# Performance work log

Measured on AMD Instinct MI355X. Metric: run time of the kernel, lower is better.

Reference implementation:

```python
import jax, jax.numpy as jnp
from jax import lax
import numpy as np

B, C, H, W = 8, 192, 56, 56
N = H * W
K_CLUSTERS = 16   # num_centroids
K_NBRS = 9        # kNN neighbors
FACTOR = 2
COUT = C * FACTOR # hidden channels of graph conv
CPE_K = 7         # depthwise CPE kernel (odd)


def setup_inputs() -> dict:
    key = jax.random.key(0)
    ks = jax.random.split(key, 12)
    s = 0.02
    return {
        "x": jax.random.normal(ks[0], (B, C, H, W), jnp.float32),
        "labels": jax.random.randint(ks[1], (B, N), 0, K_CLUSTERS, jnp.int32),
        "cpe_w": jax.random.normal(ks[2], (C, 1, CPE_K, CPE_K), jnp.float32) * s,
        "cpe_b": jnp.zeros((C,), jnp.float32),
        "fc1_w": jax.random.normal(ks[3], (C, C), jnp.float32) * s,
        "fc1_b": jnp.zeros((C,), jnp.float32),
        "nn_v_w": jax.random.normal(ks[4], (2 * C, COUT), jnp.float32) * s,
        "nn_v_b": jnp.zeros((COUT,), jnp.float32),
        "nn_c_w": jax.random.normal(ks[5], (2 * C, COUT), jnp.float32) * s,
        "nn_c_b": jnp.zeros((COUT,), jnp.float32),
        "fc2_w": jax.random.normal(ks[6], (COUT, C), jnp.float32) * s,
        "fc2_b": jnp.zeros((C,), jnp.float32),
    }


def reference(x, labels, cpe_w, cpe_b, fc1_w, fc1_b, nn_v_w, nn_v_b,
              nn_c_w, nn_c_b, fc2_w, fc2_b):
    Bx, Cx, Hx, Wx = x.shape
    n = Hx * Wx
    shortcut = x
    # --- Conditional Position Encoding: depthwise conv + residual ---
    pe = lax.conv_general_dilated(
        x, cpe_w, (1, 1), "SAME", feature_group_count=Cx,
        dimension_numbers=("NCHW", "OIHW", "NCHW"))
    x = pe + cpe_b[None, :, None, None] + x
    # --- fc1: 1x1 conv ---
    xf = jnp.einsum("bchw,cd->bdhw", x, fc1_w) + fc1_b[None, :, None, None]
    xn = xf.reshape(Bx, Cx, n).transpose(0, 2, 1)  # [B,N,C]
    # --- organize_and_map: stable sort nodes by cluster label ---
    order = jnp.argsort(labels, axis=1)            # sorted pos -> orig idx (stable)
    mapping = jnp.argsort(order, axis=1)           # orig idx -> sorted pos
    xs = jnp.take_along_axis(xn, order[:, :, None], axis=1)  # [B,N,C]
    ls = jnp.take_along_axis(labels, order, axis=1)          # [B,N]
    # --- kNN on l2-normalized feats, restricted to same cluster ---
    xe = xs / jnp.maximum(jnp.linalg.norm(xs, axis=-1, keepdims=True), 1e-12)
    sq = jnp.sum(xe * xe, axis=-1)                 # [B,N]
    d2 = sq[:, :, None] + sq[:, None, :] - 2.0 * jnp.einsum("bnc,bmc->bnm", xe, xe)
    same = ls[:, :, None] == ls[:, None, :]        # [B,N,N] cluster mask
    d2 = jnp.where(same, d2, jnp.inf)
    _, nbr = lax.top_k(-d2, K_NBRS)                # [B,N,k] nearest in-cluster
    valid = jnp.take_along_axis(same, nbr, axis=2) # False when cluster < k
    # --- vertex edge conv: max_j MLP([x_i, x_j - x_i]) ---
    xj = jax.vmap(lambda xb, nb: xb[nb])(xs, nbr)  # [B,N,k,C]
    xi = xs[:, :, None, :]
    msg = jnp.concatenate([jnp.broadcast_to(xi, xj.shape), xj - xi], axis=-1)
    h = jax.nn.gelu(msg @ nn_v_w + nn_v_b)         # [B,N,k,COUT]
    h = jnp.where(valid[..., None], h, -jnp.inf)   # self is always valid
    hv = jnp.max(h, axis=2)                        # [B,N,COUT]
    # --- centroid edge conv over cluster centers (fully connected per image) ---
    onehot = (ls[:, :, None] == jnp.arange(K_CLUSTERS)[None, None, :]).astype(xs.dtype)
    cnt = jnp.maximum(onehot.sum(axis=1), 1.0)     # [B,K]
    cen = jnp.einsum("bnk,bnc->bkc", onehot, xs) / cnt[:, :, None]
    ci = cen[:, :, None, :]
    cj = cen[:, None, :, :]
    cmsg = jnp.concatenate(
        [jnp.broadcast_to(ci, (Bx, K_CLUSTERS, K_CLUSTERS, Cx)), cj - ci], axis=-1)
    hc = jnp.max(jax.nn.gelu(cmsg @ nn_c_w + nn_c_b), axis=2)  # [B,K,COUT]
    hcn = jax.vmap(lambda hb, lb: hb[lb])(hc, ls)  # scatter center feat to nodes
    hn = hv + hcn                                  # [B,N,COUT]
    # --- unshuffle back to original raster order ---
    out_nodes = jnp.take_along_axis(hn, mapping[:, :, None], axis=1)
    # --- fc2: 1x1 conv back to C, residual ---
    y = out_nodes @ fc2_w + fc2_b                  # [B,N,C]
    y = y.transpose(0, 2, 1).reshape(Bx, Cx, Hx, Wx)
    return y + shortcut
```

## Files before the change

### kernel.cpp

```cpp
#include <hip/hip_runtime.h>
#include <math.h>

#define NB 8
#define NC 192
#define NH 56
#define NW 56
#define NN 3136
#define NK 16
#define KNB 9
#define NCOUT 384
#define LPMAX 320
#define DSTRIDE 320
#define DSLOT (320 * 320)

#define FLT_INF __builtin_inff()

typedef short s16x8 __attribute__((ext_vector_type(8)));
typedef _Float16 f16x8 __attribute__((ext_vector_type(8)));
typedef float f32x4 __attribute__((ext_vector_type(4)));
typedef unsigned short us8 __attribute__((ext_vector_type(8)));
typedef unsigned short us4 __attribute__((ext_vector_type(4)));

__device__ __forceinline__ float gelu_t(float x) {
    const float k0 = 0.7978845608028654f;
    float u = k0 * (x + 0.044715f * x * x * x);
    float sg = __builtin_amdgcn_rcpf(1.0f + __expf(-2.0f * u));
    return x * sg;
}

__device__ __forceinline__ unsigned short f2bf(float f) {
    unsigned u = __float_as_uint(f);
    u += 0x7fff + ((u >> 16) & 1);
    return (unsigned short)(u >> 16);
}

__device__ __forceinline__ float bf2f(unsigned short h) {
    return __uint_as_float(((unsigned)h) << 16);
}


#define FRONT_CONV_BLOCKS (NB * NC)
#define FRONT_ORDER_BLOCKS (NB * NK)
#define FRONT_WCVT_BLOCKS 288
__global__ __launch_bounds__(256) void front_kernel(
    const float* __restrict__ X, const float* __restrict__ W7, const float* __restrict__ bias,
    unsigned short* __restrict__ xpe,
    const int* __restrict__ labels, int* __restrict__ order, int* __restrict__ mapping,
    int* __restrict__ lsv, int* __restrict__ cntk, int* __restrict__ offk,
    const float* __restrict__ Wf1, const float* __restrict__ Wv, const float* __restrict__ Wf2,
    unsigned short* __restrict__ wf1, unsigned short* __restrict__ wfpmq,
    unsigned short* __restrict__ wfq, unsigned short* __restrict__ wf2) {
    __shared__ float tile[62 * 62];
    __shared__ float wl[49];
    int bid = blockIdx.x;
    int tid = threadIdx.x;
    if (bid < FRONT_CONV_BLOCKS) {
        int bc = (bid & 7) * NC + (bid >> 3);
        int c = bc % NC;
        const float* Xp = X + (size_t)bc * NN;
        if (tid < 49) wl[tid] = W7[(size_t)c * 49 + tid];
        for (int idx = tid; idx < 62 * 62; idx += 256) {
            int ty = idx / 62, tx = idx % 62;
            int gy = ty - 3, gx = tx - 3;
            float v = 0.0f;
            if (gy >= 0 && gy < NH && gx >= 0 && gx < NW) v = Xp[gy * NW + gx];
            tile[idx] = v;
        }
        __syncthreads();
        float cb = bias[c];
        for (int g = tid; g < (NN / 4); g += 256) {
            int y = g / (NW / 4), x0 = (g % (NW / 4)) * 4;
            float a0 = 0.f, a1 = 0.f, a2 = 0.f, a3 = 0.f;
#pragma unroll
            for (int dy = 0; dy < 7; ++dy) {
                const float* tr = &tile[(y + dy) * 62 + x0];
#pragma unroll
                for (int dx = 0; dx < 7; ++dx) {
                    float wv = wl[dy * 7 + dx];
                    a0 += tr[dx] * wv;
                    a1 += tr[dx + 1] * wv;
                    a2 += tr[dx + 2] * wv;
                    a3 += tr[dx + 3] * wv;
                }
            }
            const float* rr = &tile[(y + 3) * 62 + x0 + 3];
            us4 o;
            o[0] = f2bf(a0 + cb + rr[0]);
            o[1] = f2bf(a1 + cb + rr[1]);
            o[2] = f2bf(a2 + cb + rr[2]);
            o[3] = f2bf(a3 + cb + rr[3]);
            *(us4*)(xpe + (size_t)bc * NN + y * NW + x0) = o;
        }
    } else if (bid < FRONT_CONV_BLOCKS + FRONT_ORDER_BLOCKS) {
        if (tid >= 64) return;
        int idx = bid - FRONT_CONV_BLOCKS;
        int b = idx >> 4;
        int k = idx & 15;
        int lane = tid;
        const int* lb = labels + (size_t)b * NN;
        int cntLess = 0, cntEq = 0;
        for (int n0 = 0; n0 < NN; n0 += 64) {
            int lab = lb[n0 + lane] & 15;
            cntLess += __popcll(__ballot(lab < k));
            cntEq += __popcll(__ballot(lab == k));
        }
        int base = cntLess;
        int run = 0;
        for (int n0 = 0; n0 < NN; n0 += 64) {
            int n = n0 + lane;
            int lab = lb[n] & 15;
            bool p = (lab == k);
            unsigned long long mask = __ballot(p);
            int rank = __popcll(mask & ((1ull << lane) - 1ull));
            if (p) {
                int pos = base + run + rank;
                order[b * NN + pos] = n;
                mapping[b * NN + n] = pos;
                lsv[b * NN + pos] = k;
            }
            run += __popcll(mask);
        }
        if (lane == 0) {
            offk[b * NK + k] = base;
            cntk[b * NK + k] = cntEq;
        }
    } else {
        int u = bid - (FRONT_CONV_BLOCKS + FRONT_ORDER_BLOCKS);
        int nt = u % 6, kc = (u / 6) % 12, z = u / 72;
        const float* W;
        unsigned short* Bf;
        int ldw, rowoff, KC, NT;
        bool diff = false;
        if (z == 0) { W = Wf1; Bf = wf1; ldw = NC; rowoff = 0; KC = 6; NT = 3; }
        else if (z == 1) { W = Wv; Bf = wfpmq; ldw = NCOUT; rowoff = 0; KC = 6; NT = 6; diff = true; }
        else if (z == 2) { W = Wv; Bf = wfq; ldw = NCOUT; rowoff = NC; KC = 6; NT = 6; }
        else { W = Wf2; Bf = wf2; ldw = NC; rowoff = 0; KC = 12; NT = 3; }
        if (nt >= NT || kc >= KC) return;
        int c = tid >> 6, l = tid & 63;
        int n = l & 15, q = l >> 4;
        int col = nt * 64 + c * 16 + n;
        int krow = rowoff + kc * 32 + q * 8;
        unsigned short pack[8];
#pragma unroll
        for (int j = 0; j < 8; ++j) {
            float v = W[(size_t)(krow + j) * ldw + col];
            if (diff) v -= W[(size_t)(NC + krow + j) * ldw + col];
            pack[j] = f2bf(v);
        }
        *(us8*)(Bf + ((((size_t)nt * KC + kc) * 4 + c) * 64 + l) * 8) = *(const us8*)pack;
    }
}

__global__ __launch_bounds__(256) void fc1_kernel(const unsigned short* __restrict__ xpe,
                                                  const unsigned short* __restrict__ Bf,
                                                  const float* __restrict__ bias,
                                                  float* __restrict__ xs,
                                                  unsigned short* __restrict__ Cfrag,
                                                  const int* __restrict__ rowmap) {
    int lin = blockIdx.x;
    int b = lin & 7, by = lin >> 3;
    int w = threadIdx.x >> 6, lane = threadIdx.x & 63;
    int sg = by * 4 + w;
    int m = lane & 15, q = lane >> 4;
    int n = by * 64 + w * 16 + m;
    const unsigned short* Xb = xpe + (size_t)b * NC * NN + n;
    f32x4 acc[12] = {};
#pragma unroll
    for (int kc = 0; kc < 6; ++kc) {
        int ch = kc * 32 + q * 8;
        s16x8 a;
#pragma unroll
        for (int j = 0; j < 8; ++j) a[j] = (short)Xb[(size_t)(ch + j) * NN];
#pragma unroll
        for (int ct = 0; ct < 12; ++ct) {
            s16x8 bv = *(const s16x8*)(Bf + ((((size_t)(ct >> 2) * 6 + kc) * 4 + (ct & 3)) * 64 + lane) * 8);
            acc[ct] = __builtin_amdgcn_mfma_f32_16x16x32_bf16(a, bv, acc[ct], 0, 0, 0);
        }
    }
    float* Cb = xs + (size_t)b * NN * NC;
#pragma unroll
    for (int r = 0; r < 4; ++r) {
        int grow = sg * 16 + q * 4 + r;
        int orow = rowmap[(size_t)b * NN + grow];
        int s2 = orow >> 4, m2 = orow & 15;
#pragma unroll
        for (int ct = 0; ct < 12; ++ct) {
            int col = ct * 16 + m;
            float v = acc[ct][r] + bias[col];
            Cb[(size_t)orow * NC + col] = v;
            int kc2 = col >> 5, q2 = (col >> 3) & 3, j2 = col & 7;
            Cfrag[(size_t)b * NN * NC + (((size_t)s2 * 6 + kc2) * 64 + q2 * 16 + m2) * 8 + j2] =
                f2bf(v);
        }
    }
}

template <int KC>
__global__ __launch_bounds__(256) void gemm_mfma_pq(const unsigned short* __restrict__ Af,
                                                    size_t aStride,
                                                    const unsigned short* __restrict__ B1,
                                                    const unsigned short* __restrict__ B2,
                                                    const float* __restrict__ bias,
                                                    unsigned short* __restrict__ PmQ,
                                                    unsigned short* __restrict__ Qh,
                                                    size_t cStride, int ldc) {
    int lin = ((int)blockIdx.z * 49 + blockIdx.y) * 6 + blockIdx.x;
    int b = lin & 7, pos = lin >> 3;
    int bx = pos % 6, by = pos / 6;
    int w = threadIdx.x >> 6, lane = threadIdx.x & 63;
    int sg = by * 4 + w;
    int n0 = bx * 64;
    const unsigned short* Ap = Af + (size_t)b * aStride + ((size_t)sg * KC * 64 + lane) * 8;
    const unsigned short* Bp1 = B1 + ((size_t)bx * KC * 256 + lane) * 8;
    const unsigned short* Bp2 = B2 + ((size_t)bx * KC * 256 + lane) * 8;
    f32x4 acc1[4] = {};
    f32x4 acc2[4] = {};
#pragma unroll
    for (int kc = 0; kc < KC; ++kc) {
        s16x8 a = *(const s16x8*)(Ap + kc * 512);
#pragma unroll
        for (int c = 0; c < 4; ++c) {
            s16x8 b1 = *(const s16x8*)(Bp1 + kc * 2048 + c * 512);
            acc1[c] = __builtin_amdgcn_mfma_f32_16x16x32_bf16(a, b1, acc1[c], 0, 0, 0);
            s16x8 b2 = *(const s16x8*)(Bp2 + kc * 2048 + c * 512);
            acc2[c] = __builtin_amdgcn_mfma_f32_16x16x32_bf16(a, b2, acc2[c], 0, 0, 0);
        }
    }
    int col0 = lane & 15, rq = lane >> 4;
    unsigned short* Pb = PmQ + (size_t)b * cStride;
    unsigned short* Qb = Qh + (size_t)b * cStride;
#pragma unroll
    for (int r = 0; r < 4; ++r) {
        int grow = sg * 16 + rq * 4 + r;
#pragma unroll
        for (int c = 0; c < 4; ++c) {
            int col = n0 + c * 16 + col0;
            Pb[(size_t)grow * ldc + col] = f2bf(acc1[c][r] + bias[col]);
            Qb[(size_t)grow * ldc + col] = f2bf(acc2[c][r]);
        }
    }
}

__global__ __launch_bounds__(384) void xe_cvt_kernel(const float* __restrict__ xs,
                                                     const int* __restrict__ offk,
                                                     const int* __restrict__ cntk,
                                                     _Float16* __restrict__ xef,
                                                     float* __restrict__ sqv) {
    __shared__ float psum[16][25];
    __shared__ float rloc[16];
    int lin = ((int)blockIdx.z * 16 + blockIdx.y) * 20 + blockIdx.x;
    int b = lin & 7, pos = lin >> 3;
    int k = pos / 20, strip = pos % 20;
    int bk = b * NK + k;
    int base = offk[bk], L = cntk[bk];
    if (strip * 16 >= L) return;
    int kc = threadIdx.x >> 6, l = threadIdx.x & 63;
    int m = l & 15, q = l >> 4;
    int rl = strip * 16 + m;
    int row = base + (rl < L ? rl : L - 1);
    const float* src = xs + ((size_t)b * NN + row) * NC + kc * 32 + q * 8;
    float4 v0 = *(const float4*)src;
    float4 v1 = *(const float4*)(src + 4);
    float part = v0.x * v0.x + v0.y * v0.y + v0.z * v0.z + v0.w * v0.w + v1.x * v1.x +
                 v1.y * v1.y + v1.z * v1.z + v1.w * v1.w;
    psum[m][kc * 4 + q] = part;
    __syncthreads();
    if (threadIdx.x < 16) {
        float s = 0.0f;
#pragma unroll
        for (int i2 = 0; i2 < 24; ++i2) s += psum[threadIdx.x][i2];
        float nrm = fmaxf(sqrtf(s), 1e-12f);
        float ri = 1.0f / nrm;
        rloc[threadIdx.x] = ri;
        if (strip * 16 + (int)threadIdx.x < L)
            sqv[(size_t)b * NN + base + strip * 16 + threadIdx.x] = (s * ri) * ri;
    }
    __syncthreads();
    float rv = rloc[m];
    f16x8 pack;
    pack[0] = (_Float16)(v0.x * rv);
    pack[1] = (_Float16)(v0.y * rv);
    pack[2] = (_Float16)(v0.z * rv);
    pack[3] = (_Float16)(v0.w * rv);
    pack[4] = (_Float16)(v1.x * rv);
    pack[5] = (_Float16)(v1.y * rv);
    pack[6] = (_Float16)(v1.z * rv);
    pack[7] = (_Float16)(v1.w * rv);
    *(f16x8*)(xef + (size_t)bk * (20 * 6 * 512) + (((size_t)strip * 6 + kc) * 64 + l) * 8) =
        pack;
}

__global__ __launch_bounds__(256) void gram_kernel(const _Float16* __restrict__ xef,
                                                   const float* __restrict__ sqv,
                                                   const int* __restrict__ offk,
                                                   const int* __restrict__ cntk,
                                                   float* __restrict__ D) {
    int lin = ((int)blockIdx.z * 5 + blockIdx.y) * 5 + blockIdx.x;
    int b = lin & 7, pos = lin >> 3;
    int k = pos / 25, rr = pos % 25;
    int tj = rr / 5, ti = rr % 5;
    int bk = b * NK + k;
    int base = offk[bk], L = cntk[bk];
    if (ti * 64 >= L || tj * 64 >= L) return;
    int w = threadIdx.x >> 6, lane = threadIdx.x & 63;
    const _Float16* Xf = xef + (size_t)bk * (20 * 6 * 512);
    const _Float16* Ap = Xf + (((size_t)(ti * 4 + w) * 6) * 64 + lane) * 8;
    f32x4 acc[4] = {};
#pragma unroll
    for (int kc = 0; kc < 6; ++kc) {
        f16x8 a = *(const f16x8*)(Ap + kc * 512);
#pragma unroll
        for (int js = 0; js < 4; ++js) {
            f16x8 bv = *(const f16x8*)(Xf + (((size_t)(tj * 4 + js) * 6 + kc) * 64 + lane) * 8);
            acc[js] = __builtin_amdgcn_mfma_f32_16x16x32_f16(a, bv, acc[js], 0, 0, 0);
        }
    }
    float* Dr = D + (size_t)bk * DSLOT;
    const float* Sb = sqv + (size_t)b * NN + base;
    int col0 = lane & 15, rq = lane >> 4;
#pragma unroll
    for (int r = 0; r < 4; ++r) {
        int i = ti * 64 + w * 16 + rq * 4 + r;
        if (i >= L) continue;
        float si = Sb[i];
#pragma unroll
        for (int js = 0; js < 4; ++js) {
            int j = tj * 64 + js * 16 + col0;
            if (j < L) Dr[(size_t)i * DSTRIDE + j] = si + Sb[j] - 2.0f * acc[js][r];
        }
    }
}

#define LEXLT(da, ca, db, cb) ((da) < (db) || ((da) == (db) && (ca) < (cb)))
__global__ __launch_bounds__(256) void select9_kernel(const float* __restrict__ D,
                                                      const int* __restrict__ lsv,
                                                      const int* __restrict__ offk,
                                                      const int* __restrict__ cntk,
                                                      int* __restrict__ nbr) {
    int lin = (int)blockIdx.y * 784 + blockIdx.x;
    int b = lin & 7, quad = lin >> 3;
    int r = quad * 4 + (threadIdx.x >> 6);
    int lane = threadIdx.x & 63;
    int k = lsv[(size_t)b * NN + r];
    int bk = b * NK + k;
    int base = offk[bk], L = cntk[bk];
    int Lc = L < LPMAX ? L : LPMAX;
    const float* Dr = D + (size_t)bk * DSLOT + (size_t)(r - base) * DSTRIDE;
    float d0, d1, d2, d3, d4;
    int c0, c1, c2, c3, c4;
    c0 = lane;
    c1 = lane + 64;
    c2 = lane + 128;
    c3 = lane + 192;
    c4 = lane + 256;
    d0 = c0 < Lc ? Dr[c0] : FLT_INF;
    d1 = c1 < Lc ? Dr[c1] : FLT_INF;
    d2 = c2 < Lc ? Dr[c2] : FLT_INF;
    d3 = c3 < Lc ? Dr[c3] : FLT_INF;
    d4 = c4 < Lc ? Dr[c4] : FLT_INF;
#define CS(da, ca, db, cb)                  \
    if (LEXLT(db, cb, da, ca)) {            \
        float t = da; da = db; db = t;      \
        int u = ca; ca = cb; cb = u;        \
    }
    CS(d0, c0, d1, c1) CS(d3, c3, d4, c4) CS(d2, c2, d4, c4) CS(d2, c2, d3, c3)
    CS(d1, c1, d4, c4) CS(d0, c0, d3, c3) CS(d0, c0, d2, c2) CS(d1, c1, d3, c3)
    CS(d1, c1, d2, c2)
#undef CS
    size_t row = (size_t)b * NN + r;
    for (int q = 0; q < KNB; ++q) {
        float bd = d0;
        int bc = c0;
#pragma unroll
        for (int m = 32; m; m >>= 1) {
            float od = __shfl_xor(bd, m, 64);
            int oc = __shfl_xor(bc, m, 64);
            if (LEXLT(od, oc, bd, bc)) {
                bd = od;
                bc = oc;
            }
        }
        if (lane == 0) nbr[row * KNB + q] = base + bc;
        if (d0 == bd && c0 == bc) {
            d0 = d1; c0 = c1;
            d1 = d2; c1 = c2;
            d2 = d3; c2 = c3;
            d3 = d4; c3 = c4;
            d4 = FLT_INF; c4 = 0x7fffffff;
        }
    }
}

__global__ __launch_bounds__(768) void cenpq_kernel(const float* __restrict__ xs,
                                                    const int* __restrict__ offk,
                                                    const int* __restrict__ cntk,
                                                    const float* __restrict__ Wc,
                                                    const float* __restrict__ bc,
                                                    float* __restrict__ Pc,
                                                    float* __restrict__ Qc) {
    __shared__ float part[4][NC];
    __shared__ float ce[NC];
    __shared__ float pcs[NCOUT], qcs[NCOUT];
    int bk = ((int)blockIdx.x & 7) * NK + ((int)blockIdx.x >> 3);
    int b = bk >> 4;
    int base = offk[bk], L = cntk[bk];
    int w = threadIdx.x / NC;
    int c = threadIdx.x % NC;
    const float* Xb = xs + ((size_t)b * NN + base) * NC + c;
    float s = 0.0f;
    for (int r = w; r < L; r += 4) s += Xb[(size_t)r * NC];
    part[w][c] = s;
    __syncthreads();
    if (threadIdx.x < NC) {
        int cc = threadIdx.x;
        float tot = part[0][cc] + part[1][cc] + part[2][cc] + part[3][cc];
        ce[cc] = tot / fmaxf((float)L, 1.0f);
    }
    __syncthreads();
    int o = threadIdx.x % NCOUT, half = threadIdx.x / NCOUT;
    float pc = 0.0f, qc = 0.0f;
    int cs = half * 96, cend = cs + 96;
    for (int c2 = cs; c2 < cend; ++c2) {
        float cv = ce[c2];
        pc += cv * Wc[(size_t)c2 * NCOUT + o];
        qc += cv * Wc[(size_t)(NC + c2) * NCOUT + o];
    }
    if (half == 1) {
        pcs[o] = pc;
        qcs[o] = qc;
    }
    __syncthreads();
    if (half == 0) {
        Pc[(size_t)bk * NCOUT + o] = pc + pcs[o] + bc[o];
        Qc[(size_t)bk * NCOUT + o] = qc + qcs[o];
    }
}

__global__ __launch_bounds__(384) void hcmax_kernel(const float* __restrict__ Pc,
                                                    const float* __restrict__ Qc,
                                                    float* __restrict__ hc) {
    int bk = ((int)blockIdx.x & 7) * NK + ((int)blockIdx.x >> 3);
    int b = bk >> 4, i = bk & 15;
    int o = threadIdx.x;
    float pi = Pc[((size_t)b * NK + i) * NCOUT + o];
    float qi = Qc[((size_t)b * NK + i) * NCOUT + o];
    float pmq = pi - qi;
    float qmn = FLT_INF, qmx = -FLT_INF;
    for (int j = 0; j < NK; ++j) {
        float v = Qc[((size_t)b * NK + j) * NCOUT + o];
        qmn = fminf(qmn, v);
        qmx = fmaxf(qmx, v);
    }
    hc[((size_t)b * NK + i) * NCOUT + o] =
        fmaxf(gelu_t(pmq + qmn), gelu_t(pmq + qmx));
}

__global__ __launch_bounds__(256) void fc2hv_kernel(const unsigned short* __restrict__ PmQ,
                                                    const unsigned short* __restrict__ Qh,
                                                    const int* __restrict__ nbr,
                                                    const int* __restrict__ lsv,
                                                    const float* __restrict__ hc,
                                                    const unsigned short* __restrict__ Bf,
                                                    const float* __restrict__ bias,
                                                    unsigned short* __restrict__ C) {
    __shared__ unsigned short hn[4 * 12 * 64 * 8];
    int lin = blockIdx.x;
    int b = lin & 7, by = lin >> 3;
    int t = threadIdx.x;
    int i = t >> 2;
    int qc = t & 3;
    size_t grow = (size_t)by * 64 + i;
    size_t row = (size_t)b * NN + grow;
    int lab = lsv[row];
    int jn[KNB];
#pragma unroll
    for (int qq = 0; qq < KNB; ++qq) jn[qq] = nbr[row * KNB + qq];
    const unsigned short* Qbb = Qh + (size_t)b * NN * NCOUT;
    const unsigned short* Pr = PmQ + row * NCOUT;
    const float* hcr = hc + ((size_t)b * NK + lab) * NCOUT;
    int wq = t >> 6, mq = (t >> 2) & 15;
#pragma unroll
    for (int k = 0; k < 12; ++k) {
        int o0 = k * 32 + qc * 8;
        us8 pv = *(const us8*)(Pr + o0);
        us8 q0 = *(const us8*)(Qbb + (size_t)jn[0] * NCOUT + o0);
        float qmn[8], qmx[8];
#pragma unroll
        for (int e = 0; e < 8; ++e) {
            float v = bf2f(q0[e]);
            qmn[e] = v;
            qmx[e] = v;
        }
#pragma unroll
        for (int q = 1; q < KNB; ++q) {
            us8 qv = *(const us8*)(Qbb + (size_t)jn[q] * NCOUT + o0);
#pragma unroll
            for (int e = 0; e < 8; ++e) {
                float v = bf2f(qv[e]);
                qmn[e] = fminf(qmn[e], v);
                qmx[e] = fmaxf(qmx[e], v);
            }
        }
        float4 h0 = *(const float4*)(hcr + o0);
        float4 h1 = *(const float4*)(hcr + o0 + 4);
        float hcv[8] = {h0.x, h0.y, h0.z, h0.w, h1.x, h1.y, h1.z, h1.w};
        us8 pack;
#pragma unroll
        for (int e = 0; e < 8; ++e) {
            float pmq = bf2f(pv[e]);
            float mx = fmaxf(gelu_t(pmq + qmn[e]), gelu_t(pmq + qmx[e]));
            pack[e] = f2bf(mx + hcv[e]);
        }
        int slot = (wq * 12 + k) * 64 + qc * 16 + mq;
        *(us8*)(hn + (size_t)slot * 8) = pack;
    }
    __syncthreads();
    int w = t >> 6, lane = t & 63;
    f32x4 acc[12] = {};
#pragma unroll
    for (int kc = 0; kc < 12; ++kc) {
        s16x8 a = *(const s16x8*)(hn + (((size_t)w * 12 + kc) * 64 + lane) * 8);
#pragma unroll
        for (int ct = 0; ct < 12; ++ct) {
            s16x8 bv = *(const s16x8*)(Bf + ((((size_t)(ct >> 2) * 12 + kc) * 4 + (ct & 3)) * 64 + lane) * 8);
            acc[ct] = __builtin_amdgcn_mfma_f32_16x16x32_bf16(a, bv, acc[ct], 0, 0, 0);
        }
    }
    int col0 = lane & 15, rq = lane >> 4;
    unsigned short* Cb = C + (size_t)b * NN * NC;
    int sg = by * 4 + w;
#pragma unroll
    for (int r = 0; r < 4; ++r) {
        int grow2 = sg * 16 + rq * 4 + r;
#pragma unroll
        for (int ct = 0; ct < 12; ++ct) {
            int col = ct * 16 + col0;
            Cb[(size_t)grow2 * NC + col] = f2bf(acc[ct][r] + bias[col]);
        }
    }
}

__global__ void out_kernel(const unsigned short* __restrict__ T, const float* __restrict__ X,
                           const int* __restrict__ mapping, float* __restrict__ Y) {
    __shared__ float t[32][33];
    int lin = ((int)blockIdx.z * 98 + blockIdx.y) * 6 + blockIdx.x;
    int b = lin & 7, pos = lin >> 3;
    int c0 = (pos % 6) * 32, n0 = (pos / 6) * 32;
    int tx = threadIdx.x, ty = threadIdx.y;
#pragma unroll
    for (int q = 0; q < 4; ++q) {
        int n = n0 + ty + q * 8;
        int srow = mapping[(size_t)b * NN + n];
        t[ty + q * 8][tx] = bf2f(T[((size_t)b * NN + srow) * NC + c0 + tx]);
    }
    __syncthreads();
#pragma unroll
    for (int q = 0; q < 4; ++q) {
        int c = c0 + ty + q * 8;
        size_t idx = ((size_t)b * NC + c) * NN + n0 + tx;
        Y[idx] = t[tx][ty + q * 8] + X[idx];
    }
}

extern "C" void kernel_launch(void* const* d_in, const int* in_sizes, int n_in, void* d_out,
                              int out_size, void* d_ws, size_t ws_size, hipStream_t stream) {
    const float* x = (const float*)d_in[0];
    const int* labels = (const int*)d_in[1];
    const float* cpe_w = (const float*)d_in[2];
    const float* cpe_b = (const float*)d_in[3];
    const float* fc1_w = (const float*)d_in[4];
    const float* fc1_b = (const float*)d_in[5];
    const float* nn_v_w = (const float*)d_in[6];
    const float* nn_v_b = (const float*)d_in[7];
    const float* nn_c_w = (const float*)d_in[8];
    const float* nn_c_b = (const float*)d_in[9];
    const float* fc2_w = (const float*)d_in[10];
    const float* fc2_b = (const float*)d_in[11];
    float* out = (float*)d_out;

    const size_t SZ_XS = (size_t)NB * NN * NC;
    const size_t SZ_P = (size_t)NB * NN * NCOUT;
    const size_t BN = (size_t)NB * NN;
    const size_t SZ_CEN = (size_t)NB * NK * NC;
    const size_t SZ_PC = (size_t)NB * NK * NCOUT;

    float* base = (float*)d_ws;
    float* xs = base;
    float* xpeRegion = xs + SZ_XS;
    float* Pb = xpeRegion + SZ_XS;
    float* Qb = Pb + SZ_P;
    float* rinv = Qb + SZ_P;
    float* sqv = rinv + BN;
    float* cen = sqv + BN;
    float* Pc = cen + SZ_CEN;
    float* Qc = Pc + SZ_PC;
    float* hcv = Qc + SZ_PC;
    int* order = (int*)(hcv + SZ_PC);
    int* mapping = order + BN;
    int* lsv = mapping + BN;
    int* nbrv = lsv + BN;
    int* cntk = nbrv + BN * KNB;
    int* offk = cntk + NB * NK;
    unsigned short* xpe = (unsigned short*)xpeRegion;
    float* Dbuf = Pb;
    unsigned short* PmQh = (unsigned short*)Pb;
    unsigned short* Qh = (unsigned short*)Qb;
    unsigned short* out_t = (unsigned short*)xs;
    unsigned short* frag = (unsigned short*)(offk + NB * NK);
    unsigned short* xs_frag = frag + SZ_XS;
    unsigned short* wf1 = frag + 2 * SZ_XS;
    unsigned short* wfpmq = wf1 + (size_t)NC * NC;
    unsigned short* wfq = wfpmq + (size_t)NC * NCOUT;
    unsigned short* wf2 = wfq + (size_t)NC * NCOUT;
    _Float16* xef = (_Float16*)(wf2 + (size_t)NCOUT * NC);

    front_kernel<<<FRONT_CONV_BLOCKS + FRONT_ORDER_BLOCKS + FRONT_WCVT_BLOCKS, 256, 0, stream>>>(
        x, cpe_w, cpe_b, xpe, labels, order, mapping, lsv, cntk, offk, fc1_w, nn_v_w, fc2_w,
        wf1, wfpmq, wfq, wf2);
    fc1_kernel<<<NB * (NN / 64), 256, 0, stream>>>(xpe, wf1, fc1_b, xs, xs_frag, mapping);
    xe_cvt_kernel<<<dim3(LPMAX / 16, NK, NB), 384, 0, stream>>>(xs, offk, cntk, xef, sqv);
    gram_kernel<<<dim3(LPMAX / 64, LPMAX / 64, NB * NK), 256, 0, stream>>>(xef, sqv, offk,
                                                                           cntk, Dbuf);
    select9_kernel<<<dim3(NN / 4, NB), 256, 0, stream>>>(Dbuf, lsv, offk, cntk, nbrv);
    gemm_mfma_pq<6><<<dim3(NCOUT / 64, NN / 64, NB), 256, 0, stream>>>(
        xs_frag, SZ_XS / NB, wfpmq, wfq, nn_v_b, PmQh, Qh, (size_t)NN * NCOUT, NCOUT);
    cenpq_kernel<<<NB * NK, 768, 0, stream>>>(xs, offk, cntk, nn_c_w, nn_c_b, Pc, Qc);
    hcmax_kernel<<<NB * NK, NCOUT, 0, stream>>>(Pc, Qc, hcv);
    fc2hv_kernel<<<NB * (NN / 64), 256, 0, stream>>>(PmQh, Qh, nbrv, lsv, hcv, wf2, fc2_b,
                                                     out_t);
    out_kernel<<<dim3(NC / 32, NN / 32, NB), dim3(32, 8), 0, stream>>>(out_t, x, mapping, out);
}
```

Before: 321.7 us.

## Split fused hv+fc2 kernel and widen PQ GEMM tiles

Splits the fused neighbor-max/GELU plus fc2 MFMA kernel into a separate gather kernel (hv_kernel) that writes bf16 fragments to global memory, followed by a standalone fc2 GEMM. The hv stage now runs with many small blocks for more parallelism on the gather. The PQ GEMM is reworked so each block computes 192 output columns at once, reusing the A fragment across more MFMAs. The split adds a global round trip of the hidden tensor and an extra launch, and the wider GEMM raises register pressure.

```diff
diff --git a/kernel.cpp b/kernel.cpp
--- a/kernel.cpp
+++ b/kernel.cpp
@@ -195,48 +195,43 @@
     }
 }
 
-template <int KC>
-__global__ __launch_bounds__(256) void gemm_mfma_pq(const unsigned short* __restrict__ Af,
-                                                    size_t aStride,
-                                                    const unsigned short* __restrict__ B1,
-                                                    const unsigned short* __restrict__ B2,
-                                                    const float* __restrict__ bias,
-                                                    unsigned short* __restrict__ PmQ,
-                                                    unsigned short* __restrict__ Qh,
-                                                    size_t cStride, int ldc) {
-    int lin = ((int)blockIdx.z * 49 + blockIdx.y) * 6 + blockIdx.x;
+__global__ __launch_bounds__(256) void gemm_mfma_pq2(const unsigned short* __restrict__ Af,
+                                                     const unsigned short* __restrict__ B1,
+                                                     const unsigned short* __restrict__ B2,
+                                                     const float* __restrict__ bias,
+                                                     unsigned short* __restrict__ PmQ,
+                                                     unsigned short* __restrict__ Qh) {
+    int lin = blockIdx.x;
     int b = lin & 7, pos = lin >> 3;
-    int bx = pos % 6, by = pos / 6;
+    int half = pos & 1, by = pos >> 1;
     int w = threadIdx.x >> 6, lane = threadIdx.x & 63;
     int sg = by * 4 + w;
-    int n0 = bx * 64;
-    const unsigned short* Ap = Af + (size_t)b * aStride + ((size_t)sg * KC * 64 + lane) * 8;
-    const unsigned short* Bp1 = B1 + ((size_t)bx * KC * 256 + lane) * 8;
-    const unsigned short* Bp2 = B2 + ((size_t)bx * KC * 256 + lane) * 8;
-    f32x4 acc1[4] = {};
-    f32x4 acc2[4] = {};
-#pragma unroll
-    for (int kc = 0; kc < KC; ++kc) {
+    const unsigned short* Ap = Af + (size_t)b * NN * NC + ((size_t)sg * 6 * 64 + lane) * 8;
+    f32x4 acc1[12] = {};
+    f32x4 acc2[12] = {};
+#pragma unroll
+    for (int kc = 0; kc < 6; ++kc) {
         s16x8 a = *(const s16x8*)(Ap + kc * 512);
 #pragma unroll
-        for (int c = 0; c < 4; ++c) {
-            s16x8 b1 = *(const s16x8*)(Bp1 + kc * 2048 + c * 512);
-            acc1[c] = __builtin_amdgcn_mfma_f32_16x16x32_bf16(a, b1, acc1[c], 0, 0, 0);
-            s16x8 b2 = *(const s16x8*)(Bp2 + kc * 2048 + c * 512);
-            acc2[c] = __builtin_amdgcn_mfma_f32_16x16x32_bf16(a, b2, acc2[c], 0, 0, 0);
+        for (int ct = 0; ct < 12; ++ct) {
+            size_t boff = ((((size_t)(half * 3 + (ct >> 2)) * 6 + kc) * 4 + (ct & 3)) * 64 + lane) * 8;
+            s16x8 b1 = *(const s16x8*)(B1 + boff);
+            acc1[ct] = __builtin_amdgcn_mfma_f32_16x16x32_bf16(a, b1, acc1[ct], 0, 0, 0);
+            s16x8 b2 = *(const s16x8*)(B2 + boff);
+            acc2[ct] = __builtin_amdgcn_mfma_f32_16x16x32_bf16(a, b2, acc2[ct], 0, 0, 0);
         }
     }
     int col0 = lane & 15, rq = lane >> 4;
-    unsigned short* Pb = PmQ + (size_t)b * cStride;
-    unsigned short* Qb = Qh + (size_t)b * cStride;
+    unsigned short* Pb = PmQ + (size_t)b * NN * NCOUT;
+    unsigned short* Qb = Qh + (size_t)b * NN * NCOUT;
 #pragma unroll
     for (int r = 0; r < 4; ++r) {
         int grow = sg * 16 + rq * 4 + r;
 #pragma unroll
-        for (int c = 0; c < 4; ++c) {
-            int col = n0 + c * 16 + col0;
-            Pb[(size_t)grow * ldc + col] = f2bf(acc1[c][r] + bias[col]);
-            Qb[(size_t)grow * ldc + col] = f2bf(acc2[c][r]);
+        for (int ct = 0; ct < 12; ++ct) {
+            int col = half * 192 + ct * 16 + col0;
+            Pb[(size_t)grow * NCOUT + col] = f2bf(acc1[ct][r] + bias[col]);
+            Qb[(size_t)grow * NCOUT + col] = f2bf(acc2[ct][r]);
         }
     }
 }
@@ -455,87 +450,93 @@
         fmaxf(gelu_t(pmq + qmn), gelu_t(pmq + qmx));
 }
 
-__global__ __launch_bounds__(256) void fc2hv_kernel(const unsigned short* __restrict__ PmQ,
-                                                    const unsigned short* __restrict__ Qh,
-                                                    const int* __restrict__ nbr,
-                                                    const int* __restrict__ lsv,
-                                                    const float* __restrict__ hc,
+__global__ __launch_bounds__(192) void hv_kernel(const unsigned short* __restrict__ PmQ,
+                                                 const unsigned short* __restrict__ Qh,
+                                                 const int* __restrict__ nbr,
+                                                 const int* __restrict__ lsv,
+                                                 const float* __restrict__ hc,
+                                                 unsigned short* __restrict__ hnf) {
+    int lin = (int)blockIdx.y * 784 + blockIdx.x;
+    int b = lin & 7, quad = lin >> 3;
+    int t = threadIdx.x;
+    int rsub = t / 48, c = t % 48;
+    int i = quad * 4 + rsub;
+    size_t row = (size_t)b * NN + i;
+    int lab = lsv[row];
+    int o0 = c * 8;
+    int jn[KNB];
+#pragma unroll
+    for (int q = 0; q < KNB; ++q) jn[q] = nbr[row * KNB + q];
+    const unsigned short* Qbb = Qh + (size_t)b * NN * NCOUT + o0;
+    us8 pv = *(const us8*)(PmQ + row * NCOUT + o0);
+    us8 q0 = *(const us8*)(Qbb + (size_t)jn[0] * NCOUT);
+    float qmn[8], qmx[8];
+#pragma unroll
+    for (int e = 0; e < 8; ++e) {
+        float v = bf2f(q0[e]);
+        qmn[e] = v;
+        qmx[e] = v;
+    }
+#pragma unroll
+    for (int q = 1; q < KNB; ++q) {
+        us8 qv = *(const us8*)(Qbb + (size_t)jn[q] * NCOUT);
+#pragma unroll
+        for (int e = 0; e < 8; ++e) {
+            float v = bf2f(qv[e]);
+            qmn[e] = fminf(qmn[e], v);
+            qmx[e] = fmaxf(qmx[e], v);
+        }
+    }
+    const float* hcr = hc + ((size_t)b * NK + lab) * NCOUT + o0;
+    float4 h0 = *(const float4*)hcr;
+    float4 h1 = *(const float4*)(hcr + 4);
+    float hcv[8] = {h0.x, h0.y, h0.z, h0.w, h1.x, h1.y, h1.z, h1.w};
+    unsigned short pack[8];
+#pragma unroll
+    for (int e = 0; e < 8; ++e) {
+        float pmq = bf2f(pv[e]);
+        float m = fmaxf(gelu_t(pmq + qmn[e]), gelu_t(pmq + qmx[e]));
+        pack[e] = f2bf(m + hcv[e]);
+    }
+    int s = i >> 4, mm = i & 15;
+    *(us8*)(hnf + (size_t)b * NN * NCOUT +
+            (((size_t)s * 12 + (c >> 2)) * 64 + (c & 3) * 16 + mm) * 8) = *(const us8*)pack;
+}
+
+template <int KC>
+__global__ __launch_bounds__(256) void gemm_mfma_hb(const unsigned short* __restrict__ Af,
+                                                    size_t aStride,
                                                     const unsigned short* __restrict__ Bf,
                                                     const float* __restrict__ bias,
-                                                    unsigned short* __restrict__ C) {
-    __shared__ unsigned short hn[4 * 12 * 64 * 8];
-    int lin = blockIdx.x;
-    int b = lin & 7, by = lin >> 3;
-    int t = threadIdx.x;
-    int i = t >> 2;
-    int qc = t & 3;
-    size_t grow = (size_t)by * 64 + i;
-    size_t row = (size_t)b * NN + grow;
-    int lab = lsv[row];
-    int jn[KNB];
-#pragma unroll
-    for (int qq = 0; qq < KNB; ++qq) jn[qq] = nbr[row * KNB + qq];
-    const unsigned short* Qbb = Qh + (size_t)b * NN * NCOUT;
-    const unsigned short* Pr = PmQ + row * NCOUT;
-    const float* hcr = hc + ((size_t)b * NK + lab) * NCOUT;
-    int wq = t >> 6, mq = (t >> 2) & 15;
-#pragma unroll
-    for (int k = 0; k < 12; ++k) {
-        int o0 = k * 32 + qc * 8;
-        us8 pv = *(const us8*)(Pr + o0);
-        us8 q0 = *(const us8*)(Qbb + (size_t)jn[0] * NCOUT + o0);
-        float qmn[8], qmx[8];
-#pragma unroll
-        for (int e = 0; e < 8; ++e) {
-            float v = bf2f(q0[e]);
-            qmn[e] = v;
-            qmx[e] = v;
-        }
-#pragma unroll
-        for (int q = 1; q < KNB; ++q) {
-            us8 qv = *(const us8*)(Qbb + (size_t)jn[q] * NCOUT + o0);
-#pragma unroll
-            for (int e = 0; e < 8; ++e) {
-                float v = bf2f(qv[e]);
-                qmn[e] = fminf(qmn[e], v);
-                qmx[e] = fmaxf(qmx[e], v);
-            }
-        }
-        float4 h0 = *(const float4*)(hcr + o0);
-        float4 h1 = *(const float4*)(hcr + o0 + 4);
-        float hcv[8] = {h0.x, h0.y, h0.z, h0.w, h1.x, h1.y, h1.z, h1.w};
-        us8 pack;
-#pragma unroll
-        for (int e = 0; e < 8; ++e) {
-            float pmq = bf2f(pv[e]);
-            float mx = fmaxf(gelu_t(pmq + qmn[e]), gelu_t(pmq + qmx[e]));
-            pack[e] = f2bf(mx + hcv[e]);
-        }
-        int slot = (wq * 12 + k) * 64 + qc * 16 + mq;
-        *(us8*)(hn + (size_t)slot * 8) = pack;
-    }
-    __syncthreads();
-    int w = t >> 6, lane = t & 63;
-    f32x4 acc[12] = {};
-#pragma unroll
-    for (int kc = 0; kc < 12; ++kc) {
-        s16x8 a = *(const s16x8*)(hn + (((size_t)w * 12 + kc) * 64 + lane) * 8);
-#pragma unroll
-        for (int ct = 0; ct < 12; ++ct) {
-            s16x8 bv = *(const s16x8*)(Bf + ((((size_t)(ct >> 2) * 12 + kc) * 4 + (ct & 3)) * 64 + lane) * 8);
-            acc[ct] = __builtin_amdgcn_mfma_f32_16x16x32_bf16(a, bv, acc[ct], 0, 0, 0);
+                                                    unsigned short* __restrict__ C,
+                                                    size_t cStride, int ldc) {
+    int lin = ((int)blockIdx.z * 49 + blockIdx.y) * 3 + blockIdx.x;
+    int b = lin & 7, pos = lin >> 3;
+    int bx = pos % 3, by = pos / 3;
+    int w = threadIdx.x >> 6, lane = threadIdx.x & 63;
+    int sg = by * 4 + w;
+    int n0 = bx * 64;
+    const unsigned short* Ap = Af + (size_t)b * aStride + ((size_t)sg * KC * 64 + lane) * 8;
+    const unsigned short* Bp = Bf + ((size_t)bx * KC * 256 + lane) * 8;
+    f32x4 acc[4] = {};
+#pragma unroll
+    for (int kc = 0; kc < KC; ++kc) {
+        s16x8 a = *(const s16x8*)(Ap + kc * 512);
+#pragma unroll
+        for (int c = 0; c < 4; ++c) {
+            s16x8 bv = *(const s16x8*)(Bp + kc * 2048 + c * 512);
+            acc[c] = __builtin_amdgcn_mfma_f32_16x16x32_bf16(a, bv, acc[c], 0, 0, 0);
         }
     }
     int col0 = lane & 15, rq = lane >> 4;
-    unsigned short* Cb = C + (size_t)b * NN * NC;
-    int sg = by * 4 + w;
+    unsigned short* Cb = C + (size_t)b * cStride;
 #pragma unroll
     for (int r = 0; r < 4; ++r) {
-        int grow2 = sg * 16 + rq * 4 + r;
-#pragma unroll
-        for (int ct = 0; ct < 12; ++ct) {
-            int col = ct * 16 + col0;
-            Cb[(size_t)grow2 * NC + col] = f2bf(acc[ct][r] + bias[col]);
+        int grow = sg * 16 + rq * 4 + r;
+#pragma unroll
+        for (int c = 0; c < 4; ++c) {
+            int col = n0 + c * 16 + col0;
+            Cb[(size_t)grow * ldc + col] = f2bf(acc[c][r] + bias[col]);
         }
     }
 }
@@ -607,6 +608,7 @@
     unsigned short* Qh = (unsigned short*)Qb;
     unsigned short* out_t = (unsigned short*)xs;
     unsigned short* frag = (unsigned short*)(offk + NB * NK);
+    unsigned short* hn_frag = frag;
     unsigned short* xs_frag = frag + SZ_XS;
     unsigned short* wf1 = frag + 2 * SZ_XS;
     unsigned short* wfpmq = wf1 + (size_t)NC * NC;
@@ -622,11 +624,12 @@
     gram_kernel<<<dim3(LPMAX / 64, LPMAX / 64, NB * NK), 256, 0, stream>>>(xef, sqv, offk,
                                                                            cntk, Dbuf);
     select9_kernel<<<dim3(NN / 4, NB), 256, 0, stream>>>(Dbuf, lsv, offk, cntk, nbrv);
-    gemm_mfma_pq<6><<<dim3(NCOUT / 64, NN / 64, NB), 256, 0, stream>>>(
-        xs_frag, SZ_XS / NB, wfpmq, wfq, nn_v_b, PmQh, Qh, (size_t)NN * NCOUT, NCOUT);
+    gemm_mfma_pq2<<<NB * 2 * (NN / 64), 256, 0, stream>>>(xs_frag, wfpmq, wfq, nn_v_b, PmQh,
+                                                          Qh);
     cenpq_kernel<<<NB * NK, 768, 0, stream>>>(xs, offk, cntk, nn_c_w, nn_c_b, Pc, Qc);
     hcmax_kernel<<<NB * NK, NCOUT, 0, stream>>>(Pc, Qc, hcv);
-    fc2hv_kernel<<<NB * (NN / 64), 256, 0, stream>>>(PmQh, Qh, nbrv, lsv, hcv, wf2, fc2_b,
-                                                     out_t);
+    hv_kernel<<<dim3(NN / 4, NB), 192, 0, stream>>>(PmQh, Qh, nbrv, lsv, hcv, hn_frag);
+    gemm_mfma_hb<12><<<dim3(NC / 64, NN / 64, NB), 256, 0, stream>>>(
+        hn_frag, SZ_P / NB, wf2, fc2_b, out_t, (size_t)NN * NC, NC);
     out_kernel<<<dim3(NC / 32, NN / 32, NB), dim3(32, 8), 0, stream>>>(out_t, x, mapping, out);
 }
```

New measurement: 331.8 us. +3.1%, slower.
